# Kernel tuning notes

Measured on AMD Instinct MI355X. Metric: run time of the kernel, lower is better.

The kernel has to match this reference:

```python
import jax, jax.numpy as jnp
import numpy as np

B, S, D, H = 4, 1024, 1024, 16
DK = D // H  # 64


def setup_inputs() -> dict:
    key = jax.random.key(0)
    ks = jax.random.split(key, 12)
    scale = 0.02
    inp = {
        "query": jax.random.normal(ks[0], (B, S, D), jnp.float32),
        "key": jax.random.normal(ks[1], (B, S, D), jnp.float32),
        "value": jax.random.normal(ks[2], (B, S, D), jnp.float32),
        "mask": jax.random.randint(ks[3], (B, 1, S, S), 0, 2, jnp.int32),
        "wq": jax.random.normal(ks[4], (D, D), jnp.float32) * scale,
        "bq": jnp.zeros((D,), jnp.float32),
        "wk": jax.random.normal(ks[5], (D, D), jnp.float32) * scale,
        "bk": jnp.zeros((D,), jnp.float32),
        "wv": jax.random.normal(ks[6], (D, D), jnp.float32) * scale,
        "bv": jnp.zeros((D,), jnp.float32),
        "wo": jax.random.normal(ks[7], (D, D), jnp.float32) * scale,
        "bo": jnp.zeros((D,), jnp.float32),
    }
    return inp


def reference(query, key, value, mask, wq, bq, wk, bk, wv, bv, wo, bo):
    # Linear projections (torch Linear: x @ W.T + b)
    q = query @ wq.T + bq
    k = key @ wk.T + bk
    v = value @ wv.T + bv
    # [B,S,D] -> [B,H,S,DK]
    q = q.reshape(B, S, H, DK).transpose(0, 2, 1, 3)
    k = k.reshape(B, S, H, DK).transpose(0, 2, 1, 3)
    v = v.reshape(B, S, H, DK).transpose(0, 2, 1, 3)
    # scaled dot-product attention with mask (-1e9 where mask==0)
    scores = jnp.einsum('bhqd,bhkd->bhqk', q, k) / jnp.sqrt(jnp.float32(DK))
    scores = jnp.where(mask == 0, jnp.float32(-1e9), scores)
    attn = jax.nn.softmax(scores, axis=-1)  # dropout p=0.0 -> identity
    x = jnp.einsum('bhqk,bhkd->bhqd', attn, v)
    # [B,H,S,DK] -> [B,S,D]
    x = x.transpose(0, 2, 1, 3).reshape(B, S, D)
    return x @ wo.T + bo
```

## Files before the change

### kernel.cpp

```cpp
#include <hip/hip_runtime.h>


typedef __attribute__((ext_vector_type(8))) short short8;
typedef __attribute__((ext_vector_type(4))) float f32x4;
typedef __attribute__((ext_vector_type(4))) unsigned short u16x4;
typedef unsigned short u16;
typedef unsigned long long u64;

#define SCALE_Q 0.180336880f

__device__ __forceinline__ u16 f2bf(float f) {
    unsigned u = __float_as_uint(f);
    return (u16)((u + 0x7FFFu + ((u >> 16) & 1u)) >> 16);
}
__device__ __forceinline__ u16 f2bf_fast(float f) {
    return (u16)((__float_as_uint(f) + 0x8000u) >> 16);
}
__device__ __forceinline__ float bf2f(u16 v) {
    return __uint_as_float((unsigned)v << 16);
}

__device__ __forceinline__ void gl_lds16(const u16* g, u16* l) {
    __builtin_amdgcn_global_load_lds(
        (__attribute__((address_space(1))) void*)g,
        (__attribute__((address_space(3))) void*)l, 16, 0, 0);
}

__global__ __launch_bounds__(256) void prep(
    const float* __restrict__ q, const float* __restrict__ k,
    const float* __restrict__ v, const float* __restrict__ wq,
    const float* __restrict__ wk, const float* __restrict__ wv,
    const float* __restrict__ wo, const int* __restrict__ mask,
    u16* __restrict__ xq, u16* __restrict__ xk, u16* __restrict__ xv,
    u16* __restrict__ wqb, u16* __restrict__ wkb, u16* __restrict__ wvb,
    u16* __restrict__ wob, u64* __restrict__ bits) {
    int bid = blockIdx.x;
    if (bid < 16384) {
        const float* src; u16* dst; int i;
        if (bid < 12288) {
            int chunk = bid >> 12;
            int off = bid & 4095;
            src = (chunk == 0) ? q : ((chunk == 1) ? k : v);
            dst = (chunk == 0) ? xq : ((chunk == 1) ? xk : xv);
            i = off * 256 + threadIdx.x;
        } else {
            int wb = bid - 12288;
            int chunk = wb >> 10;
            int off = wb & 1023;
            src = (chunk == 0) ? wq : ((chunk == 1) ? wk : ((chunk == 2) ? wv : wo));
            dst = (chunk == 0) ? wqb : ((chunk == 1) ? wkb : ((chunk == 2) ? wvb : wob));
            i = off * 256 + threadIdx.x;
        }
        f32x4 val = ((const f32x4*)src)[i];
        u16x4 r;
        r.x = f2bf(val.x); r.y = f2bf(val.y); r.z = f2bf(val.z); r.w = f2bf(val.w);
        ((u16x4*)dst)[i] = r;
    } else {
        int mb = bid - 16384;
        int wid = threadIdx.x >> 6, lane = threadIdx.x & 63;
        int base = mb * 1024 + wid * 256;
        int b = mb >> 10, qrow = mb & 1023;
        #pragma unroll
        for (int j = 0; j < 4; ++j) {
            u64 bal = __ballot(mask[base + j * 64 + lane] != 0);
            int kt = wid * 4 + j;
            if (lane == 0) bits[(size_t)(b * 16 + kt) * 1024 + qrow] = bal;
        }
    }
}

__global__ __launch_bounds__(256, 3) void gemm_qkv(
    const u16* __restrict__ Aq, const u16* __restrict__ Ak, const u16* __restrict__ Av,
    const u16* __restrict__ Wq, const u16* __restrict__ Wk, const u16* __restrict__ Wv,
    const float* __restrict__ bq, const float* __restrict__ bk, const float* __restrict__ bv,
    u16* __restrict__ Qo, u16* __restrict__ Ko, u16* __restrict__ VTo) {
    __shared__ __align__(16) u16 As[128 * 64];
    __shared__ __align__(16) u16 Bs[128 * 64];
    const int id = blockIdx.x;
    const int n0 = (id / 96) * 128;
    const int pm = id % 96;
    const int p = pm >> 5;
    const int m0 = (pm & 31) * 128;
    const u16* A = (p == 0) ? Aq : ((p == 1) ? Ak : Av);
    const u16* W = (p == 0) ? Wq : ((p == 1) ? Wk : Wv);
    const float* bias = (p == 0) ? bq : ((p == 1) ? bk : bv);

    const int t = threadIdx.x;
    const int lane = t & 63;
    const int wid = t >> 6;
    const int l15 = lane & 15;
    const int quad = lane >> 4;
    const int wm = (wid & 1) * 64;
    const int wn = (wid >> 1) * 64;
    const int r8 = lane >> 3, gr = lane & 7;
    const int gsw = (gr ^ r8) * 8;

    f32x4 acc[4][4];
    #pragma unroll
    for (int i = 0; i < 4; ++i)
        #pragma unroll
        for (int j = 0; j < 4; ++j) acc[i][j] = (f32x4){0.f, 0.f, 0.f, 0.f};

    for (int kt = 0; kt < 1024; kt += 64) {
        __syncthreads();
        #pragma unroll
        for (int c = 0; c < 8; ++c) {
            int call = wid * 8 + c;
            if (call < 16) {
                int rb = call * 8;
                gl_lds16(&A[(size_t)(m0 + rb + r8) * 1024 + kt + gsw], &As[rb * 64]);
            } else {
                int rb = (call - 16) * 8;
                gl_lds16(&W[(size_t)(n0 + rb + r8) * 1024 + kt + gsw], &Bs[rb * 64]);
            }
        }
        __syncthreads();
        #pragma unroll
        for (int ks = 0; ks < 2; ++ks) {
            short8 af[4], bf[4];
            #pragma unroll
            for (int i = 0; i < 4; ++i) {
                int mr = wm + i * 16 + l15;
                af[i] = *(const short8*)&As[mr * 64 + (((ks << 2) + quad) ^ (mr & 7)) * 8];
                int nr = wn + i * 16 + l15;
                bf[i] = *(const short8*)&Bs[nr * 64 + (((ks << 2) + quad) ^ (nr & 7)) * 8];
            }
            #pragma unroll
            for (int mi = 0; mi < 4; ++mi)
                #pragma unroll
                for (int ni = 0; ni < 4; ++ni)
                    acc[mi][ni] = __builtin_amdgcn_mfma_f32_16x16x32_bf16(
                        af[mi], bf[ni], acc[mi][ni], 0, 0, 0);
        }
    }

    u16* dst01 = (p == 0) ? Qo : Ko;
    const float qs = (p == 0) ? SCALE_Q : 1.0f;
    #pragma unroll
    for (int mi = 0; mi < 4; ++mi) {
        #pragma unroll
        for (int ni = 0; ni < 4; ++ni) {
            int col = n0 + wn + ni * 16 + l15;
            int h = col >> 6, dk = col & 63;
            float bcol = bias[col];
            if (p < 2) {
                #pragma unroll
                for (int r = 0; r < 4; ++r) {
                    int row = m0 + wm + mi * 16 + quad * 4 + r;
                    int bb = row >> 10, s = row & 1023;
                    dst01[(size_t)((bb * 16 + h) * 1024 + s) * 64 + dk] =
                        f2bf((acc[mi][ni][r] + bcol) * qs);
                }
            } else {
                int row0 = m0 + wm + mi * 16 + quad * 4;
                int bb = row0 >> 10, s0 = row0 & 1023;
                u64 pk = 0;
                #pragma unroll
                for (int r = 0; r < 4; ++r)
                    pk |= (u64)f2bf(acc[mi][ni][r] + bcol) << (16 * r);
                *(u64*)&VTo[(size_t)((bb * 16 + h) * 64 + dk) * 1024 + s0] = pk;
            }
        }
    }
}

__global__ __launch_bounds__(256, 3) void gemm_out(
    const u16* __restrict__ X, const u16* __restrict__ Wo,
    const float* __restrict__ bo, float* __restrict__ out) {
    __shared__ __align__(16) u16 As[64 * 64];
    __shared__ __align__(16) u16 Bs[128 * 64];
    const int id = blockIdx.x;
    const int n0 = (id >> 6) * 128;
    const int m0 = (id & 63) * 64;
    const int t = threadIdx.x;
    const int lane = t & 63;
    const int wid = t >> 6;
    const int l15 = lane & 15;
    const int quad = lane >> 4;
    const int wm = (wid & 1) * 32;
    const int wn = (wid >> 1) * 64;
    const int r8 = lane >> 3, gr = lane & 7;
    const int gsw = (gr ^ r8) * 8;

    f32x4 acc[2][4];
    #pragma unroll
    for (int i = 0; i < 2; ++i)
        #pragma unroll
        for (int j = 0; j < 4; ++j) acc[i][j] = (f32x4){0.f, 0.f, 0.f, 0.f};

    for (int kt = 0; kt < 1024; kt += 64) {
        __syncthreads();
        #pragma unroll
        for (int c = 0; c < 6; ++c) {
            int call = wid * 6 + c;
            if (call < 8) {
                int rb = call * 8;
                gl_lds16(&X[(size_t)(m0 + rb + r8) * 1024 + kt + gsw], &As[rb * 64]);
            } else {
                int rb = (call - 8) * 8;
                gl_lds16(&Wo[(size_t)(n0 + rb + r8) * 1024 + kt + gsw], &Bs[rb * 64]);
            }
        }
        __syncthreads();
        #pragma unroll
        for (int ks = 0; ks < 2; ++ks) {
            short8 af[2], bf[4];
            #pragma unroll
            for (int i = 0; i < 2; ++i) {
                int mr = wm + i * 16 + l15;
                af[i] = *(const short8*)&As[mr * 64 + (((ks << 2) + quad) ^ (mr & 7)) * 8];
            }
            #pragma unroll
            for (int j = 0; j < 4; ++j) {
                int nr = wn + j * 16 + l15;
                bf[j] = *(const short8*)&Bs[nr * 64 + (((ks << 2) + quad) ^ (nr & 7)) * 8];
            }
            #pragma unroll
            for (int mi = 0; mi < 2; ++mi)
                #pragma unroll
                for (int ni = 0; ni < 4; ++ni)
                    acc[mi][ni] = __builtin_amdgcn_mfma_f32_16x16x32_bf16(
                        af[mi], bf[ni], acc[mi][ni], 0, 0, 0);
        }
    }

    #pragma unroll
    for (int mi = 0; mi < 2; ++mi) {
        #pragma unroll
        for (int ni = 0; ni < 4; ++ni) {
            int col = n0 + wn + ni * 16 + l15;
            float bcol = bo[col];
            #pragma unroll
            for (int r = 0; r < 4; ++r) {
                int row = m0 + wm + mi * 16 + quad * 4 + r;
                out[(size_t)row * 1024 + col] = acc[mi][ni][r] + bcol;
            }
        }
    }
}

__global__ __launch_bounds__(256) void attn_kernel(
    const u16* __restrict__ Q, const u16* __restrict__ K, const u16* __restrict__ VT,
    const u64* __restrict__ mbits, u16* __restrict__ O, float* __restrict__ L) {
    __shared__ __align__(16) u16 Ks[64 * 64];
    __shared__ __align__(16) u16 Vs[64 * 64];
    __shared__ __align__(16) u16 Ps[4][16 * 72];

    const int qt = blockIdx.x;
    const int h = blockIdx.y;
    const int b = blockIdx.z >> 1;
    const int half = blockIdx.z & 1;
    const int t = threadIdx.x;
    const int lane = t & 63;
    const int wid = t >> 6;
    const int l15 = lane & 15;
    const int quad = lane >> 4;
    const int q0 = qt * 64;
    const int sr = t >> 3;
    const int sc = t & 7;
    const int ktg0 = half * 8;

    const size_t headoff = (size_t)(b * 16 + h) * 1024 * 64;
    const u16* Qh = Q + headoff;
    const u16* Kh = K + headoff;
    const u16* Vh = VT + headoff;

    short8 qf[2];
    #pragma unroll
    for (int ks = 0; ks < 2; ++ks)
        qf[ks] = *(const short8*)&Qh[(size_t)(q0 + wid * 16 + l15) * 64 + ks * 32 + quad * 8];

    f32x4 o_acc[4];
    #pragma unroll
    for (int j = 0; j < 4; ++j) o_acc[j] = (f32x4){0.f, 0.f, 0.f, 0.f};
    float lacc = 0.f;

    const u64* mbase = &mbits[(size_t)(b * 16) * 1024 + q0 + wid * 16 + l15];

    short8 kpre[2], vpre[2];
    #pragma unroll
    for (int p = 0; p < 2; ++p) {
        int r = p * 32 + sr;
        kpre[p] = *(const short8*)&Kh[(size_t)(ktg0 * 64 + r) * 64 + sc * 8];
        vpre[p] = *(const short8*)&Vh[(size_t)r * 1024 + ktg0 * 64 + sc * 8];
    }

    for (int kt = 0; kt < 8; ++kt) {
        __syncthreads();
        #pragma unroll
        for (int p = 0; p < 2; ++p) {
            int r = p * 32 + sr;
            int gl = sc ^ (r & 7);
            *(short8*)&Ks[r * 64 + gl * 8] = kpre[p];
            *(short8*)&Vs[r * 64 + gl * 8] = vpre[p];
        }
        __syncthreads();

        if (kt < 7) {
            int kvn = (ktg0 + kt + 1) * 64;
            #pragma unroll
            for (int p = 0; p < 2; ++p) {
                int r = p * 32 + sr;
                kpre[p] = *(const short8*)&Kh[(size_t)(kvn + r) * 64 + sc * 8];
                vpre[p] = *(const short8*)&Vh[(size_t)r * 1024 + kvn + sc * 8];
            }
        }

        f32x4 sacc[4];
        #pragma unroll
        for (int j = 0; j < 4; ++j) sacc[j] = (f32x4){0.f, 0.f, 0.f, 0.f};
        #pragma unroll
        for (int ks = 0; ks < 2; ++ks) {
            #pragma unroll
            for (int mi = 0; mi < 4; ++mi) {
                int n = mi * 16 + l15;
                short8 kf = *(const short8*)&Ks[n * 64 + (((ks << 2) + quad) ^ (n & 7)) * 8];
                sacc[mi] = __builtin_amdgcn_mfma_f32_16x16x32_bf16(kf, qf[ks], sacc[mi], 0, 0, 0);
            }
        }

        u64 w = mbase[(size_t)(ktg0 + kt) * 1024];
        unsigned t0 = (unsigned)(w >> (quad * 4));
        unsigned t1 = (unsigned)(w >> (quad * 4 + 32));
        #pragma unroll
        for (int mi = 0; mi < 4; ++mi) {
            unsigned sel = (mi & 2) ? t1 : t0;
            sel >>= (mi & 1) * 16;
            u64 pk = 0;
            #pragma unroll
            for (int r = 0; r < 4; ++r) {
                float p = __builtin_amdgcn_exp2f(sacc[mi][r]);
                p = ((sel >> r) & 1u) ? p : 0.f;
                lacc += p;
                pk |= (u64)f2bf_fast(p) << (16 * r);
            }
            *(u64*)&Ps[wid][l15 * 72 + mi * 16 + quad * 4] = pk;
        }

        #pragma unroll
        for (int ks = 0; ks < 2; ++ks) {
            short8 pf = *(const short8*)&Ps[wid][l15 * 72 + ks * 32 + quad * 8];
            #pragma unroll
            for (int j = 0; j < 4; ++j) {
                int d = j * 16 + l15;
                short8 vf = *(const short8*)&Vs[d * 64 + (((ks << 2) + quad) ^ (d & 7)) * 8];
                o_acc[j] = __builtin_amdgcn_mfma_f32_16x16x32_bf16(pf, vf, o_acc[j], 0, 0, 0);
            }
        }
    }

    float l = lacc;
    l += __shfl_xor(l, 16);
    l += __shfl_xor(l, 32);
    u16* Oh = O + (size_t)half * 4194304;
    float* Lh = L + (size_t)half * 65536;
    if (lane < 16)
        Lh[(size_t)(b * 16 + h) * 1024 + q0 + wid * 16 + lane] = l;
    #pragma unroll
    for (int r = 0; r < 4; ++r) {
        int qrow = q0 + wid * 16 + quad * 4 + r;
        #pragma unroll
        for (int ni = 0; ni < 4; ++ni) {
            Oh[(size_t)(b * 1024 + qrow) * 1024 + h * 64 + ni * 16 + l15] =
                f2bf(o_acc[ni][r]);
        }
    }
}

__global__ __launch_bounds__(256) void merge_halves(
    const u16* __restrict__ O, const float* __restrict__ L, u16* __restrict__ X) {
    int i = (blockIdx.x * 256 + threadIdx.x) * 8;
    int b = i >> 20, s = (i >> 10) & 1023, c = i & 1023, h = c >> 6;
    short8 o0 = *(const short8*)&O[i];
    short8 o1 = *(const short8*)&O[4194304 + i];
    size_t li = (size_t)(b * 16 + h) * 1024 + s;
    float inv = 1.0f / (L[li] + L[65536 + li]);
    short8 r;
    #pragma unroll
    for (int j = 0; j < 8; ++j) {
        float x = (bf2f((u16)o0[j]) + bf2f((u16)o1[j])) * inv;
        r[j] = (short)f2bf(x);
    }
    *(short8*)&X[i] = r;
}

extern "C" void kernel_launch(void* const* d_in, const int* in_sizes, int n_in,
                              void* d_out, int out_size, void* d_ws, size_t ws_size,
                              hipStream_t stream) {
    const float* query = (const float*)d_in[0];
    const float* key_ = (const float*)d_in[1];
    const float* value = (const float*)d_in[2];
    const int* mask = (const int*)d_in[3];
    const float* wq = (const float*)d_in[4];
    const float* bq = (const float*)d_in[5];
    const float* wk = (const float*)d_in[6];
    const float* bk = (const float*)d_in[7];
    const float* wv = (const float*)d_in[8];
    const float* bv = (const float*)d_in[9];
    const float* wo = (const float*)d_in[10];
    const float* bo = (const float*)d_in[11];
    float* out = (float*)d_out;

    char* ws = (char*)d_ws;
    const size_t XB = (size_t)4096 * 1024 * 2;
    const size_t WB = (size_t)1024 * 1024 * 2;
    u16* xq = (u16*)(ws);
    u16* xk = (u16*)(ws + XB);
    u16* xv = (u16*)(ws + 2 * XB);
    u16* wqb = (u16*)(ws + 3 * XB);
    u16* wkb = (u16*)(ws + 3 * XB + WB);
    u16* wvb = (u16*)(ws + 3 * XB + 2 * WB);
    u16* wob = (u16*)(ws + 3 * XB + 3 * WB);
    u16* Qb = (u16*)(ws + 3 * XB + 4 * WB);
    u16* Kb = (u16*)(ws + 4 * XB + 4 * WB);
    u16* VTb = (u16*)(ws + 5 * XB + 4 * WB);
    u64* bits = (u64*)(ws + 6 * XB + 4 * WB);
    float* Lbuf = (float*)(ws + 6 * XB + 4 * WB + (512 << 10));
    u16* Opart = xk;
    u16* Xattn = xq;

    prep<<<20480, 256, 0, stream>>>(query, key_, value, wq, wk, wv, wo, mask,
                                    xq, xk, xv, wqb, wkb, wvb, wob, bits);
    gemm_qkv<<<768, 256, 0, stream>>>(xq, xk, xv, wqb, wkb, wvb,
                                      bq, bk, bv, Qb, Kb, VTb);
    attn_kernel<<<dim3(16, 16, 8), 256, 0, stream>>>(Qb, Kb, VTb, bits, Opart, Lbuf);
    merge_halves<<<2048, 256, 0, stream>>>(Opart, Lbuf, Xattn);
    gemm_out<<<512, 256, 0, stream>>>(Xattn, wob, bo, out);
}
```

Measured before the change: 231.2 us.

## Process two 16-row query groups per wave in attention kernel

Each wave now handles 32 query rows instead of 16, so every K and V fragment read from LDS feeds two MFMAs, and each block covers 128 queries. The grid is halved along the query-tile axis, which halves the K/V global loads and LDS staging per query. The cost is more registers per thread (doubled accumulators and Q fragments) and half as many blocks (1024), which may lower occupancy and latency hiding.

```diff
diff --git a/kernel.cpp b/kernel.cpp
--- a/kernel.cpp
+++ b/kernel.cpp
@@ -244,7 +244,7 @@
     const u64* __restrict__ mbits, u16* __restrict__ O, float* __restrict__ L) {
     __shared__ __align__(16) u16 Ks[64 * 64];
     __shared__ __align__(16) u16 Vs[64 * 64];
-    __shared__ __align__(16) u16 Ps[4][16 * 72];
+    __shared__ __align__(16) u16 Ps[4][32 * 72];
 
     const int qt = blockIdx.x;
     const int h = blockIdx.y;
@@ -255,7 +255,7 @@
     const int wid = t >> 6;
     const int l15 = lane & 15;
     const int quad = lane >> 4;
-    const int q0 = qt * 64;
+    const int qw = qt * 128 + wid * 32;
     const int sr = t >> 3;
     const int sc = t & 7;
     const int ktg0 = half * 8;
@@ -265,17 +265,21 @@
     const u16* Kh = K + headoff;
     const u16* Vh = VT + headoff;
 
-    short8 qf[2];
-    #pragma unroll
-    for (int ks = 0; ks < 2; ++ks)
-        qf[ks] = *(const short8*)&Qh[(size_t)(q0 + wid * 16 + l15) * 64 + ks * 32 + quad * 8];
-
-    f32x4 o_acc[4];
-    #pragma unroll
-    for (int j = 0; j < 4; ++j) o_acc[j] = (f32x4){0.f, 0.f, 0.f, 0.f};
-    float lacc = 0.f;
-
-    const u64* mbase = &mbits[(size_t)(b * 16) * 1024 + q0 + wid * 16 + l15];
+    short8 qf[2][2];
+    #pragma unroll
+    for (int g = 0; g < 2; ++g)
+        #pragma unroll
+        for (int ks = 0; ks < 2; ++ks)
+            qf[g][ks] = *(const short8*)&Qh[(size_t)(qw + g * 16 + l15) * 64 + ks * 32 + quad * 8];
+
+    f32x4 o_acc[2][4];
+    #pragma unroll
+    for (int g = 0; g < 2; ++g)
+        #pragma unroll
+        for (int j = 0; j < 4; ++j) o_acc[g][j] = (f32x4){0.f, 0.f, 0.f, 0.f};
+    float lacc[2] = {0.f, 0.f};
+
+    const u64* mbase = &mbits[(size_t)(b * 16) * 1024 + qw + l15];
 
     short8 kpre[2], vpre[2];
     #pragma unroll
@@ -306,63 +310,74 @@
             }
         }
 
-        f32x4 sacc[4];
-        #pragma unroll
-        for (int j = 0; j < 4; ++j) sacc[j] = (f32x4){0.f, 0.f, 0.f, 0.f};
+        f32x4 sacc[2][4];
+        #pragma unroll
+        for (int g = 0; g < 2; ++g)
+            #pragma unroll
+            for (int j = 0; j < 4; ++j) sacc[g][j] = (f32x4){0.f, 0.f, 0.f, 0.f};
         #pragma unroll
         for (int ks = 0; ks < 2; ++ks) {
             #pragma unroll
             for (int mi = 0; mi < 4; ++mi) {
                 int n = mi * 16 + l15;
                 short8 kf = *(const short8*)&Ks[n * 64 + (((ks << 2) + quad) ^ (n & 7)) * 8];
-                sacc[mi] = __builtin_amdgcn_mfma_f32_16x16x32_bf16(kf, qf[ks], sacc[mi], 0, 0, 0);
-            }
-        }
-
-        u64 w = mbase[(size_t)(ktg0 + kt) * 1024];
-        unsigned t0 = (unsigned)(w >> (quad * 4));
-        unsigned t1 = (unsigned)(w >> (quad * 4 + 32));
-        #pragma unroll
-        for (int mi = 0; mi < 4; ++mi) {
-            unsigned sel = (mi & 2) ? t1 : t0;
-            sel >>= (mi & 1) * 16;
-            u64 pk = 0;
-            #pragma unroll
-            for (int r = 0; r < 4; ++r) {
-                float p = __builtin_amdgcn_exp2f(sacc[mi][r]);
-                p = ((sel >> r) & 1u) ? p : 0.f;
-                lacc += p;
-                pk |= (u64)f2bf_fast(p) << (16 * r);
-            }
-            *(u64*)&Ps[wid][l15 * 72 + mi * 16 + quad * 4] = pk;
+                sacc[0][mi] = __builtin_amdgcn_mfma_f32_16x16x32_bf16(kf, qf[0][ks], sacc[0][mi], 0, 0, 0);
+                sacc[1][mi] = __builtin_amdgcn_mfma_f32_16x16x32_bf16(kf, qf[1][ks], sacc[1][mi], 0, 0, 0);
+            }
+        }
+
+        #pragma unroll
+        for (int g = 0; g < 2; ++g) {
+            u64 w = mbase[(size_t)(ktg0 + kt) * 1024 + g * 16];
+            unsigned t0 = (unsigned)(w >> (quad * 4));
+            unsigned t1 = (unsigned)(w >> (quad * 4 + 32));
+            #pragma unroll
+            for (int mi = 0; mi < 4; ++mi) {
+                unsigned sel = (mi & 2) ? t1 : t0;
+                sel >>= (mi & 1) * 16;
+                u64 pk = 0;
+                #pragma unroll
+                for (int r = 0; r < 4; ++r) {
+                    float p = __builtin_amdgcn_exp2f(sacc[g][mi][r]);
+                    p = ((sel >> r) & 1u) ? p : 0.f;
+                    lacc[g] += p;
+                    pk |= (u64)f2bf_fast(p) << (16 * r);
+                }
+                *(u64*)&Ps[wid][(g * 16 + l15) * 72 + mi * 16 + quad * 4] = pk;
+            }
         }
 
         #pragma unroll
         for (int ks = 0; ks < 2; ++ks) {
-            short8 pf = *(const short8*)&Ps[wid][l15 * 72 + ks * 32 + quad * 8];
+            short8 pf0 = *(const short8*)&Ps[wid][(size_t)l15 * 72 + ks * 32 + quad * 8];
+            short8 pf1 = *(const short8*)&Ps[wid][(size_t)(16 + l15) * 72 + ks * 32 + quad * 8];
             #pragma unroll
             for (int j = 0; j < 4; ++j) {
                 int d = j * 16 + l15;
                 short8 vf = *(const short8*)&Vs[d * 64 + (((ks << 2) + quad) ^ (d & 7)) * 8];
-                o_acc[j] = __builtin_amdgcn_mfma_f32_16x16x32_bf16(pf, vf, o_acc[j], 0, 0, 0);
-            }
-        }
-    }
-
-    float l = lacc;
-    l += __shfl_xor(l, 16);
-    l += __shfl_xor(l, 32);
+                o_acc[0][j] = __builtin_amdgcn_mfma_f32_16x16x32_bf16(pf0, vf, o_acc[0][j], 0, 0, 0);
+                o_acc[1][j] = __builtin_amdgcn_mfma_f32_16x16x32_bf16(pf1, vf, o_acc[1][j], 0, 0, 0);
+            }
+        }
+    }
+
     u16* Oh = O + (size_t)half * 4194304;
     float* Lh = L + (size_t)half * 65536;
-    if (lane < 16)
-        Lh[(size_t)(b * 16 + h) * 1024 + q0 + wid * 16 + lane] = l;
-    #pragma unroll
-    for (int r = 0; r < 4; ++r) {
-        int qrow = q0 + wid * 16 + quad * 4 + r;
-        #pragma unroll
-        for (int ni = 0; ni < 4; ++ni) {
-            Oh[(size_t)(b * 1024 + qrow) * 1024 + h * 64 + ni * 16 + l15] =
-                f2bf(o_acc[ni][r]);
+    #pragma unroll
+    for (int g = 0; g < 2; ++g) {
+        float l = lacc[g];
+        l += __shfl_xor(l, 16);
+        l += __shfl_xor(l, 32);
+        if (lane < 16)
+            Lh[(size_t)(b * 16 + h) * 1024 + qw + g * 16 + lane] = l;
+        #pragma unroll
+        for (int r = 0; r < 4; ++r) {
+            int qrow = qw + g * 16 + quad * 4 + r;
+            #pragma unroll
+            for (int ni = 0; ni < 4; ++ni) {
+                Oh[(size_t)(b * 1024 + qrow) * 1024 + h * 64 + ni * 16 + l15] =
+                    f2bf(o_acc[g][ni][r]);
+            }
         }
     }
 }
@@ -423,7 +438,7 @@
                                     xq, xk, xv, wqb, wkb, wvb, wob, bits);
     gemm_qkv<<<768, 256, 0, stream>>>(xq, xk, xv, wqb, wkb, wvb,
                                       bq, bk, bv, Qb, Kb, VTb);
-    attn_kernel<<<dim3(16, 16, 8), 256, 0, stream>>>(Qb, Kb, VTb, bits, Opart, Lbuf);
+    attn_kernel<<<dim3(8, 16, 8), 256, 0, stream>>>(Qb, Kb, VTb, bits, Opart, Lbuf);
     merge_halves<<<2048, 256, 0, stream>>>(Opart, Lbuf, Xattn);
     gemm_out<<<512, 256, 0, stream>>>(Xattn, wob, bo, out);
 }
```

Result: no change. 233.8 us (+1.1%).
